# Kernel optimization log

Hardware: AMD Instinct MI355X
Metric: run time of the kernel (lower is better)

## Reference

```python
import jax, jax.numpy as jnp
import numpy as np

B, J, I = 16, 96, 96
E, H = 256, 512
VS, VT = 32000, 32000
MAX_JUMP = 96
SJ = 2 * MAX_JUMP + 1  # 193
ALPHA_P0 = 0.3


def _lstm(x, W, b, reverse=False):
    """TF LSTMCell (gate order i, j, f, o; forget_bias=1.0). x: [B,J,E] -> [B,J,H]."""
    h_dim = W.shape[1] // 4
    xs = jnp.swapaxes(x, 0, 1)  # [J,B,E]
    if reverse:
        xs = xs[::-1]

    def step(carry, xt):
        h, c = carry
        z = jnp.concatenate([xt, h], axis=-1) @ W + b  # [B,4H]
        i, g, f, o = jnp.split(z, 4, axis=-1)
        c = jax.nn.sigmoid(f + 1.0) * c + jax.nn.sigmoid(i) * jnp.tanh(g)
        h = jax.nn.sigmoid(o) * jnp.tanh(c)
        return (h, c), h

    init = (jnp.zeros((x.shape[0], h_dim), x.dtype), jnp.zeros((x.shape[0], h_dim), x.dtype))
    _, hs = jax.lax.scan(step, init, xs)
    if reverse:
        hs = hs[::-1]
    return jnp.swapaxes(hs, 0, 1)


def setup_inputs() -> dict:
    key = jax.random.key(0)
    ks = jax.random.split(key, 16)
    s = 0.05
    return {
        "sources": jax.random.randint(ks[0], (B, I), 0, VS, dtype=jnp.int32),
        "targets": jax.random.randint(ks[1], (B, J), 0, VT, dtype=jnp.int32),
        "targets_null": jnp.array([VT - 1], dtype=jnp.int32),
        "emb": jax.random.normal(ks[2], (VT, E), jnp.float32) * s,
        "W_fw": jax.random.normal(ks[3], (E + H, 4 * H), jnp.float32) * s,
        "b_fw": jnp.zeros((4 * H,), jnp.float32),
        "W_bw": jax.random.normal(ks[4], (E + H, 4 * H), jnp.float32) * s,
        "b_bw": jnp.zeros((4 * H,), jnp.float32),
        "W_lstm": jax.random.normal(ks[5], (2 * H, E), jnp.float32) * s,
        "W1": jax.random.normal(ks[6], (E, H), jnp.float32) * s,
        "b1": jnp.zeros((H,), jnp.float32),
        "Wv": jax.random.normal(ks[7], (H, VS), jnp.float32) * s,
        "bv": jnp.zeros((VS,), jnp.float32),
        "Wj": jax.random.normal(ks[8], (H, SJ), jnp.float32) * s,
        "bj": jnp.zeros((SJ,), jnp.float32),
        "Wp": jax.random.normal(ks[9], (H, 1), jnp.float32) * s,
        "bp": jnp.zeros((1,), jnp.float32),
    }


def reference(sources, targets, targets_null, emb, W_fw, b_fw, W_bw, b_bw,
              W_lstm, W1, b1, Wv, bv, Wj, bj, Wp, bp):
    # shared target encoder (emission & transition use the same variables)
    e_word = emb[targets]          # [B,J,E]
    e_null = emb[targets_null]     # [1,E]
    h_fw = _lstm(e_word, W_fw, b_fw, reverse=False)
    h_bw = _lstm(e_word, W_bw, b_bw, reverse=True)
    ts = jnp.concatenate([h_fw, h_bw], axis=-1) @ W_lstm   # [B,J,E]
    ts = jnp.tanh(ts @ W1 + b1)                            # [B,J,H]
    tn = jnp.tanh(e_null @ W1 + b1)                        # [1,H]
    # keep_prob = 1.0 -> dropout is identity

    # ---- emission ----
    p_word = jax.nn.softmax(ts @ Wv + bv, axis=-1)         # [B,J,VS]
    p_null = jax.nn.softmax(tn @ Wv + bv, axis=-1)         # [1,VS]
    em_word = jnp.take_along_axis(p_word, sources[:, None, :], axis=2)  # [B,J,I]
    em_null = jnp.broadcast_to(p_null[0][sources][:, None, :], em_word.shape)  # tile over J
    emission_prob = jnp.concatenate([em_word, em_null], axis=1)  # [B,2J,I]

    # ---- transition ----
    jw = jax.nn.softmax(ts @ Wj + bj, axis=-1)             # [B,J,SJ]
    p0_scalar = jax.nn.sigmoid(tn @ Wp + bp)[0, 0] * ALPHA_P0
    p0 = jnp.broadcast_to(p0_scalar, (targets.shape[0], targets.shape[1]))  # [B,J]

    j_idx = jnp.arange(J)
    # window indices: for target word j, gather jw[j, MAX_JUMP - j + i] for i in [0,J)
    idx = MAX_JUMP - j_idx[:, None] + j_idx[None, :]       # [J,J]
    jww = jnp.take_along_axis(jw, idx[None, :, :], axis=2)  # [B,J,J]
    jww_sum = jnp.sum(jww, axis=-1, keepdims=True)
    jww_n = jww * (1.0 - p0[:, :, None]) / jww_sum          # normalized non-null jumps

    eye = jnp.eye(J, dtype=jww.dtype)
    half = jnp.concatenate([jww_n, p0[:, :, None] * eye], axis=2)       # [B,J,2J]
    transition = jnp.concatenate([half, half], axis=1)                  # [B,2J,2J]
    lhalf = jnp.concatenate([jnp.log(jww_n), jnp.log(p0)[:, :, None] * eye], axis=2)
    transition_log = jnp.concatenate([lhalf, lhalf], axis=1)            # [B,2J,2J]

    return emission_prob, transition, transition_log
```

## Files before the change

kernel.cpp:

```cpp
#include <hip/hip_runtime.h>
#include <math.h>

#define B_ 16
#define J_ 96
#define I_ 96
#define E_ 256
#define H_ 512
#define VS_ 32000
#define SJ_ 193
#define NROW (B_*J_)

typedef __attribute__((ext_vector_type(8))) short short8;
typedef __attribute__((ext_vector_type(4))) float f32x4;
typedef __attribute__((ext_vector_type(4))) unsigned int u32x4;

__device__ __forceinline__ float sigf(float x){ return 1.f/(1.f+__expf(-x)); }

__device__ __forceinline__ unsigned short f2bf(float x){
  unsigned int u = __float_as_uint(x);
  unsigned int r = (u + 0x7FFFu + ((u>>16)&1u)) >> 16;
  return (unsigned short)r;
}
__device__ __forceinline__ float bf2f(unsigned short u){
  return __uint_as_float((unsigned int)u << 16);
}

#define ASYNC16(gp, lp) __builtin_amdgcn_global_load_lds( \
    (const __attribute__((address_space(1))) unsigned int*)(gp), \
    (__attribute__((address_space(3))) unsigned int*)(lp), 16, 0, 0)

__device__ __forceinline__ void wtr_tile256(const float* __restrict__ src,
                                            unsigned short* __restrict__ dst,
                                            int ldN, int nmax, int K, int n0, int k0,
                                            float* __restrict__ tile )
{
  const int t = threadIdx.x;
  #pragma unroll
  for (int rep = 0; rep < 16; rep++){
    int idx = rep*256 + t;
    int kk = idx >> 6, nn = idx & 63;
    tile[kk*65 + nn] = (n0+nn < nmax) ? src[(long long)(k0+kk)*ldN + n0 + nn] : 0.f;
  }
  __syncthreads();
  #pragma unroll
  for (int rep = 0; rep < 16; rep++){
    int idx = rep*256 + t;
    int nn = idx >> 6, kk = idx & 63;
    dst[(long long)(n0+nn)*K + k0 + kk] = f2bf(tile[kk*65 + nn]);
  }
}

__device__ __forceinline__ void wtr_tile(const float* __restrict__ src,
                                         unsigned short* __restrict__ dst,
                                         int ldN, int nmax, int K, int n0, int k0,
                                         float* __restrict__ tile)
{
  const int t = threadIdx.x;
  #pragma unroll
  for (int rep = 0; rep < 8; rep++){
    int idx = rep*512 + t;
    int kk = idx >> 6, nn = idx & 63;
    tile[kk*65 + nn] = (n0+nn < nmax) ? src[(long long)(k0+kk)*ldN + n0 + nn] : 0.f;
  }
  __syncthreads();
  #pragma unroll
  for (int rep = 0; rep < 8; rep++){
    int idx = rep*512 + t;
    int nn = idx >> 6, kk = idx & 63;
    dst[(long long)(n0+nn)*K + k0 + kk] = f2bf(tile[kk*65 + nn]);
  }
}

__global__ __launch_bounds__(256) void k_head(
    const int* __restrict__ targets, const float* __restrict__ emb,
    unsigned short* __restrict__ e_word_h,
    const float* __restrict__ Wfw, const float* __restrict__ Wbw,
    unsigned short* __restrict__ WT,
    unsigned int* __restrict__ hex, float* __restrict__ rowsum,
    const float* __restrict__ bfw, const float* __restrict__ bbw,
    float* __restrict__ wsb)
{
  __shared__ float tile[64*65];
  int bid = blockIdx.x;
  const int t = threadIdx.x;
  if (bid < 1536){
    int tr = targets[bid];
    e_word_h[(long long)bid*E_ + t] = f2bf(emb[(long long)tr*E_ + t]);
    return;
  }
  bid -= 1536;
  if (bid < 256){
    int y = bid >> 7;
    const float* src = y ? Wbw : Wfw;
    unsigned short* dst = WT + (long long)y*2048*256;
    int sid = bid & 127;
    wtr_tile256(src, dst, 2048, 2048, 256, (sid & 31)*64, (sid >> 5)*64, tile);
    return;
  }
  bid -= 256;
  if (bid < 128){ hex[bid*256 + t] = 0u; return; }
  bid -= 128;
  if (bid < 7){
    int i = bid*256 + t;
    if (i < NROW + 1) rowsum[i] = 0.f;
    return;
  }
  bid -= 7;
  int i = bid*256 + t;
  wsb[i] = (i < 2048) ? bfw[i] : bbw[i - 2048];
}

__device__ __forceinline__ void gemm128(const unsigned short* __restrict__ Ah,
                                        const unsigned short* __restrict__ Bh,
                                        int K, int m0, int n0,
                                        unsigned short* As, unsigned short* Bs,
                                        f32x4 (&acc)[4][4])
{
  const int t = threadIdx.x;
  const int lane = t & 63, w = t >> 6;
  const int wm = (w >> 1)*64, wn = (w & 1)*64;
  for (int k0 = 0; k0 < K; k0 += 64){
    #pragma unroll
    for (int p = 0; p < 4; p++){
      int rowA = p*32 + (t >> 3);
      int kc = (t & 7) ^ (rowA & 7);
      const unsigned short* ga = Ah + (long long)(m0 + rowA)*K + k0 + kc*8;
      const unsigned short* gb = Bh + (long long)(n0 + rowA)*K + k0 + kc*8;
      unsigned short* la = As + p*2048 + w*512;
      unsigned short* lb = Bs + p*2048 + w*512;
      ASYNC16(ga, la);
      ASYNC16(gb, lb);
    }
    __syncthreads();
    const int rr = lane & 15, kch = lane >> 4;
    #pragma unroll
    for (int kk = 0; kk < 2; kk++){
      short8 af[4], bf[4];
      #pragma unroll
      for (int mi = 0; mi < 4; mi++){
        int rowA = wm + mi*16 + rr;
        int slot = (kk*4 + kch) ^ (rowA & 7);
        af[mi] = *(const short8*)&As[rowA*64 + slot*8];
      }
      #pragma unroll
      for (int ni = 0; ni < 4; ni++){
        int rowB = wn + ni*16 + rr;
        int slot = (kk*4 + kch) ^ (rowB & 7);
        bf[ni] = *(const short8*)&Bs[rowB*64 + slot*8];
      }
      #pragma unroll
      for (int mi = 0; mi < 4; mi++)
        #pragma unroll
        for (int ni = 0; ni < 4; ni++)
          acc[mi][ni] = __builtin_amdgcn_mfma_f32_16x16x32_bf16(af[mi], bf[ni], acc[mi][ni], 0, 0, 0);
    }
    __syncthreads();
  }
}

template<int MODE>
__global__ __launch_bounds__(256, 2) void k_bgemm(
    const unsigned short* __restrict__ Ah,
    const unsigned short* __restrict__ Bh,
    int K, int ncols,
    const float* __restrict__ bias,
    float* __restrict__ Cf,
    unsigned short* __restrict__ Ch,
    int ldc,
    long long sB2, long long sBias2, long long sC2)
{
  __shared__ unsigned short As[128*64];
  __shared__ unsigned short Bs[128*64];
  if (blockIdx.y){
    Bh += sB2;
    if (bias) bias += sBias2;
    if (Cf) Cf += sC2;
    if (Ch) Ch += sC2;
  }
  int nwg = gridDim.x;
  int braw = blockIdx.x;
  int wg = (braw & 7)*(nwg >> 3) + (braw >> 3);
  int mt = wg % 12, nt = wg / 12;
  const int m0 = mt*128, n0 = nt*128;
  f32x4 acc[4][4] = {};
  gemm128(Ah, Bh, K, m0, n0, As, Bs, acc);
  const int t = threadIdx.x;
  const int lane = t & 63, w = t >> 6;
  const int wm = (w >> 1)*64, wn = (w & 1)*64;
  #pragma unroll
  for (int mi = 0; mi < 4; mi++){
    #pragma unroll
    for (int r = 0; r < 4; r++){
      int row = m0 + wm + mi*16 + ((lane >> 4) << 2) + r;
      #pragma unroll
      for (int ni = 0; ni < 4; ni++){
        int col = n0 + wn + ni*16 + (lane & 15);
        if (col >= ncols) continue;
        float v = acc[mi][ni][r] + (bias ? bias[col] : 0.f);
        if (MODE == 0){ Cf[(long long)row*ldc + col] = v; }
        if (MODE == 1){ Ch[(long long)row*ldc + col] = f2bf(v); }
        if (MODE == 2){
          v = tanhf(v);
          if (Cf) Cf[(long long)row*ldc + col] = v;
          Ch[(long long)row*ldc + col] = f2bf(v);
        }
      }
    }
  }
}

__global__ __launch_bounds__(512, 1) void k_fused(
    const unsigned short* __restrict__ Xh,
    const float* __restrict__ Wfw, const float* __restrict__ Wbw,
    unsigned int* __restrict__ hex32,
    unsigned short* __restrict__ Hcat_h,
    const int* __restrict__ tnull, const float* __restrict__ emb,
    const float* __restrict__ W1, const float* __restrict__ b1,
    const float* __restrict__ Wp, const float* __restrict__ bp,
    const float* __restrict__ Wv, const float* __restrict__ bv,
    unsigned short* __restrict__ WvT,
    float* __restrict__ lognull, float* __restrict__ nullsum,
    float* __restrict__ p0,
    const float* __restrict__ Wl, unsigned short* __restrict__ W_comboT,
    const float* __restrict__ Wj, unsigned short* __restrict__ WjT)
{
  __shared__ __align__(16) unsigned short W_s[64*512];
  __shared__ __align__(16) float z_s[2][8][16][68];
  const int bid = blockIdx.x;
  const int t = threadIdx.x;

  if (bid >= 64){
    float* zflat = &z_s[0][0][0][0];
    int sid = bid - 64;
    if (sid == 0){
      float* en  = zflat;
      float* red = zflat + 256;
      if (t < E_) en[t] = emb[(long long)tnull[0]*E_ + t];
      __syncthreads();
      float s = b1[t];
      for (int e = 0; e < E_; e++) s += en[e]*W1[(long long)e*H_ + t];
      red[t] = tanhf(s)*Wp[t];
      __syncthreads();
      for (int w = 256; w > 0; w >>= 1){
        if (t < w) red[t] += red[t+w];
        __syncthreads();
      }
      if (t == 0) p0[0] = sigf(red[0] + bp[0])*0.3f;
      return;
    }
    sid -= 1;
    if (sid < 128){
      const int K8 = sid*8;
      float* WlS = zflat;
      #pragma unroll
      for (int rep = 0; rep < 4; rep++){
        int id = rep*512 + t;
        int kl = id >> 8, e = id & 255;
        WlS[kl*256 + e] = Wl[(long long)(K8 + kl)*256 + e];
      }
      __syncthreads();
      float acc[8] = {};
      for (int e = 0; e < 256; e++){
        float w1v = W1[(long long)e*512 + t];
        #pragma unroll
        for (int j = 0; j < 8; j++) acc[j] += WlS[j*256 + e]*w1v;
      }
      #pragma unroll
      for (int j = 0; j < 8; j++)
        W_comboT[(long long)t*1024 + K8 + j] = f2bf(acc[j]);
      return;
    }
    sid -= 128;
    if (sid < 32){
      wtr_tile(Wj, WjT, SJ_, SJ_, 512, (sid & 3)*64, (sid >> 2)*64, zflat);
      return;
    }
    sid -= 32;
    if (sid < 63){
      float* en  = zflat;
      float* tns = zflat + 256;
      float* red = zflat + 768;
      if (t < E_) en[t] = emb[(long long)tnull[0]*E_ + t];
      __syncthreads();
      float s0 = b1[t];
      for (int e = 0; e < E_; e++) s0 += en[e]*W1[(long long)e*H_ + t];
      tns[t] = tanhf(s0);
      __syncthreads();
      int c = sid*512 + t;
      float p = 0.f;
      if (c < VS_){
        float s = bv[c];
        for (int k = 0; k < H_; k++) s += tns[k]*Wv[(long long)k*VS_ + c];
        lognull[c] = s;
        p = __expf(s);
      }
      red[t] = p;
      __syncthreads();
      for (int w = 256; w > 0; w >>= 1){
        if (t < w) red[t] += red[t+w];
        __syncthreads();
      }
      if (t == 0) atomicAdd(nullsum, red[0]);
      return;
    }
    sid -= 63;
    wtr_tile(Wv, WvT, VS_, VS_, H_, (sid % 500)*64, (sid / 500)*64, zflat);
    return;
  }

  const int dir = bid >> 5;
  const int slice = bid & 31;
  const int u0 = slice * 16;
  const int lane = t & 63;
  const int w = t >> 6;
  const int m = lane & 15, hi = lane >> 4;
  const unsigned short* X = Xh + (long long)dir*NROW*2048;
  const float* Wg = (dir ? Wbw : Wfw) + (long long)E_*2048;
  char* hexd = (char*)hex32 + dir*65536;

  for (int rep = 0; rep < 8; rep++){
    int id = rep*512 + t;
    int k = id >> 3, col8 = (id & 7)*8;
    int g = col8 >> 4, uu0 = col8 & 15;
    const float* src = Wg + (long long)k*2048 + g*512 + u0 + uu0;
    float4 w0 = *(const float4*)src;
    float4 w1 = *(const float4*)(src + 4);
    float wv8[8] = {w0.x,w0.y,w0.z,w0.w,w1.x,w1.y,w1.z,w1.w};
    #pragma unroll
    for (int j = 0; j < 8; j++){
      int c = col8 + j;
      int byte = (c << 10) + (k << 1);
      byte ^= ((c & 7) << 4);
      *(unsigned short*)((char*)W_s + byte) = f2bf(wv8[j]);
    }
  }
  __syncthreads();

  short8 bfr[4][2];
  #pragma unroll
  for (int nt = 0; nt < 4; nt++)
    #pragma unroll
    for (int ck = 0; ck < 2; ck++){
      int col = nt*16 + m;
      int kc = 2*w + ck;
      int byte = (col << 10) + kc*64 + hi*16;
      byte ^= ((col & 7) << 4);
      bfr[nt][ck] = *(const short8*)((const char*)W_s + byte);
    }

  const int eb = t >> 4, eu = t & 15;
  float creg = 0.f;

  for (int step = 0; step < J_; step++){
    const int par = step & 1;
    const int t_eff = dir ? (J_-1-step) : step;
    float xg0=0.f, xg1=0.f, xg2=0.f, xg3=0.f;
    if (t < 256){
      const unsigned short* xr = X + ((long long)eb*J_ + t_eff)*2048 + u0 + eu;
      xg0 = bf2f(xr[0]); xg1 = bf2f(xr[512]); xg2 = bf2f(xr[1024]); xg3 = bf2f(xr[1536]);
      asm volatile("" : "+v"(xg0), "+v"(xg1), "+v"(xg2), "+v"(xg3));
    }
    const char* ap = hexd + par*32768 + m*2048 + w*256 + hi*32;
    u32x4 d0, d1, d2, d3;
    const unsigned expt = (unsigned)step;
    unsigned spin = 0;
    for (;;){
      asm volatile("global_load_dwordx4 %0, %1, off sc0 sc1" : "=v"(d0) : "v"(ap));
      asm volatile("global_load_dwordx4 %0, %1, off offset:16 sc0 sc1" : "=v"(d1) : "v"(ap));
      asm volatile("global_load_dwordx4 %0, %1, off offset:128 sc0 sc1" : "=v"(d2) : "v"(ap));
      asm volatile("global_load_dwordx4 %0, %1, off offset:144 sc0 sc1" : "=v"(d3) : "v"(ap));
      asm volatile("s_waitcnt vmcnt(0)" ::: "memory");
      unsigned bad = (d0[1]^expt)|(d0[3]^expt)|(d1[1]^expt)|(d1[3]^expt)
                   | (d2[1]^expt)|(d2[3]^expt)|(d3[1]^expt)|(d3[3]^expt);
      if (__all(bad == 0u)) break;
      if (++spin > 65536u) break;
      __builtin_amdgcn_s_sleep(1);
    }
    __builtin_amdgcn_sched_barrier(0);
    union { unsigned int u[4]; short8 s; } a0, a1;
    a0.u[0]=d0[0]; a0.u[1]=d0[2]; a0.u[2]=d1[0]; a0.u[3]=d1[2];
    a1.u[0]=d2[0]; a1.u[1]=d2[2]; a1.u[2]=d3[0]; a1.u[3]=d3[2];
    f32x4 acc[4] = {{0.f,0.f,0.f,0.f},{0.f,0.f,0.f,0.f},{0.f,0.f,0.f,0.f},{0.f,0.f,0.f,0.f}};
    #pragma unroll
    for (int nt = 0; nt < 4; nt++){
      acc[nt] = __builtin_amdgcn_mfma_f32_16x16x32_bf16(a0.s, bfr[nt][0], acc[nt], 0,0,0);
      acc[nt] = __builtin_amdgcn_mfma_f32_16x16x32_bf16(a1.s, bfr[nt][1], acc[nt], 0,0,0);
    }
    #pragma unroll
    for (int nt = 0; nt < 4; nt++)
      #pragma unroll
      for (int r = 0; r < 4; r++)
        z_s[par][w][hi*4 + r][nt*16 + m] = acc[nt][r];
    __syncthreads();
    if (t < 256){
      float z0 = xg0, z1 = xg1, z2 = xg2, z3 = xg3;
      #pragma unroll
      for (int ke = 0; ke < 8; ke++){
        z0 += z_s[par][ke][eb][eu];
        z1 += z_s[par][ke][eb][16 + eu];
        z2 += z_s[par][ke][eb][32 + eu];
        z3 += z_s[par][ke][eb][48 + eu];
      }
      creg = sigf(z2 + 1.f)*creg + sigf(z0)*tanhf(z1);
      float hh = sigf(z3)*tanhf(creg);
      unsigned int hb16 = (unsigned int)f2bf(hh);
      unsigned int nb = (unsigned int)__shfl_xor((int)hb16, 1);
      if (!(eu & 1)){
        unsigned long long pkt = (unsigned long long)((hb16 & 0xffffu) | (nb << 16))
                               | ((unsigned long long)(unsigned)(step+1) << 32);
        __hip_atomic_store((unsigned long long*)(hexd + (par^1)*32768 + eb*2048 + (u0 + eu)*4),
                           pkt, __ATOMIC_RELAXED, __HIP_MEMORY_SCOPE_AGENT);
      }
      Hcat_h[((long long)eb*J_ + t_eff)*1024 + dir*512 + u0 + eu] = (unsigned short)hb16;
    }
  }
}

__global__ __launch_bounds__(256, 2) void k_mega(
    const unsigned short* __restrict__ t1h,
    const unsigned short* __restrict__ WvT,
    const unsigned short* __restrict__ WjT,
    const float* __restrict__ bv, const float* __restrict__ bj,
    const int* __restrict__ sources,
    float* __restrict__ rowsum, float* __restrict__ jlog,
    float* __restrict__ out_em)
{
  __shared__ unsigned short As[128*64];
  __shared__ unsigned short Bs[128*64];
  const int t = threadIdx.x;
  const int lane = t & 63, w = t >> 6;
  int bid = blockIdx.x;
  if (bid >= 3024){
    int tile = (bid - 3024)*4 + w;
    int b = tile / 36, tl = tile % 36;
    int mt = tl / 6, nt = tl % 6;
    const int rr = lane & 15, kq = lane >> 4;
    int s = sources[b*96 + nt*16 + rr];
    float bg = bv[s];
    const unsigned short* arow = t1h + ((long long)(b*96 + mt*16 + rr))*512 + kq*8;
    const unsigned short* brow = WvT + (long long)s*512 + kq*8;
    f32x4 acc = {0.f,0.f,0.f,0.f};
    #pragma unroll
    for (int kc = 0; kc < 16; kc++){
      short8 af = *(const short8*)(arow + kc*32);
      short8 bf = *(const short8*)(brow + kc*32);
      acc = __builtin_amdgcn_mfma_f32_16x16x32_bf16(af, bf, acc, 0, 0, 0);
    }
    #pragma unroll
    for (int r = 0; r < 4; r++){
      int j = mt*16 + kq*4 + r;
      int i = nt*16 + rr;
      out_em[((long long)b*192 + j)*96 + i] = __expf(acc[r] + bg);
    }
    return;
  }
  const bool isjl = (bid >= 3000);
  int m0, n0;
  const unsigned short* Bh;
  if (isjl){
    int idx = bid - 3000;
    m0 = (idx % 12)*128; n0 = (idx / 12)*128;
    Bh = WjT;
  } else {
    int wg = (bid & 7)*375 + (bid >> 3);
    m0 = (wg % 12)*128; n0 = (wg / 12)*128;
    Bh = WvT;
  }
  f32x4 acc[4][4] = {};
  gemm128(t1h, Bh, H_, m0, n0, As, Bs, acc);
  const int wm = (w >> 1)*64, wn = (w & 1)*64;
  #pragma unroll
  for (int mi = 0; mi < 4; mi++){
    #pragma unroll
    for (int r = 0; r < 4; r++){
      int row = m0 + wm + mi*16 + ((lane >> 4) << 2) + r;
      if (isjl){
        #pragma unroll
        for (int ni = 0; ni < 4; ni++){
          int col = n0 + wn + ni*16 + (lane & 15);
          if (col < SJ_) jlog[(long long)row*SJ_ + col] = acc[mi][ni][r] + bj[col];
        }
      } else {
        float s = 0.f;
        #pragma unroll
        for (int ni = 0; ni < 4; ni++){
          int col = n0 + wn + ni*16 + (lane & 15);
          s += __expf(acc[mi][ni][r] + bv[col]);
        }
        s += __shfl_xor(s, 1);
        s += __shfl_xor(s, 2);
        s += __shfl_xor(s, 4);
        s += __shfl_xor(s, 8);
        if ((lane & 15) == 0) atomicAdd(&rowsum[row], s);
      }
    }
  }
}

__global__ __launch_bounds__(128) void k_final(
    const float* __restrict__ jlog, const float* __restrict__ p0p,
    const float* __restrict__ rowsum,
    const float* __restrict__ lognull, const float* __restrict__ nullsum,
    const int* __restrict__ sources,
    float* __restrict__ out_em, float* __restrict__ T, float* __restrict__ TL)
{
  __shared__ float ex[128];
  __shared__ float red[128];
  int bx = blockIdx.x;
  int tid = threadIdx.x;
  if (bx >= NROW){
    int b = bx - NROW;
    if (tid < 96){
      int s = sources[b*96 + tid];
      float v = __expf(lognull[s]) / nullsum[0];
      for (int jj = 0; jj < 96; jj++)
        out_em[((long long)b*192 + 96 + jj)*96 + tid] = v;
    }
    return;
  }
  int b = bx / J_, j = bx % J_;
  float inv = 1.f / rowsum[bx];
  if (tid < 96)
    out_em[((long long)b*192 + j)*96 + tid] *= inv;
  float e = 0.f;
  if (tid < 96) e = __expf(jlog[(long long)bx*SJ_ + (96 - j + tid)]);
  ex[tid] = e; red[tid] = e;
  __syncthreads();
  for (int w = 64; w > 0; w >>= 1){
    if (tid < w) red[tid] += red[tid+w];
    __syncthreads();
  }
  float p0 = p0p[0];
  float scale = (1.f - p0) / red[0];
  float lp0 = logf(p0);
  long long r0 = ((long long)b*192 + j)*192;
  long long r1 = ((long long)b*192 + j + 96)*192;
  for (int col = tid; col < 192; col += 128){
    float tv, lv;
    if (col < 96){ tv = ex[col]*scale; lv = logf(tv); }
    else { bool d = (col - 96) == j; tv = d ? p0 : 0.f; lv = d ? lp0 : 0.f; }
    T[r0 + col] = tv; T[r1 + col] = tv;
    TL[r0 + col] = lv; TL[r1 + col] = lv;
  }
}

extern "C" void kernel_launch(void* const* d_in, const int* in_sizes, int n_in,
                              void* d_out, int out_size, void* d_ws, size_t ws_size,
                              hipStream_t stream)
{
  const int* sources = (const int*)d_in[0];
  const int* targets = (const int*)d_in[1];
  const int* tnull   = (const int*)d_in[2];
  const float* emb   = (const float*)d_in[3];
  const float* Wfw   = (const float*)d_in[4];
  const float* bfw   = (const float*)d_in[5];
  const float* Wbw   = (const float*)d_in[6];
  const float* bbw   = (const float*)d_in[7];
  const float* Wl    = (const float*)d_in[8];
  const float* W1    = (const float*)d_in[9];
  const float* b1    = (const float*)d_in[10];
  const float* Wv    = (const float*)d_in[11];
  const float* bv    = (const float*)d_in[12];
  const float* Wj    = (const float*)d_in[13];
  const float* bj    = (const float*)d_in[14];
  const float* Wp    = (const float*)d_in[15];
  const float* bp    = (const float*)d_in[16];
  float* out = (float*)d_out;
  float* ws  = (float*)d_ws;

  long long off = 0;
  unsigned short* Xh = (unsigned short*)(ws + off); off += 2LL*NROW*2048/2;
  unsigned short* e_word_h = (unsigned short*)(ws + off); off += (long long)NROW*E_/2;
  unsigned short* WT       = (unsigned short*)(ws + off); off += 2LL*2048*256/2;
  unsigned short* Hcat_h   = (unsigned short*)(ws + off); off += (long long)NROW*1024/2;
  unsigned int* hex32 = (unsigned int*)(ws + off); off += 32768;
  unsigned short* t1h = (unsigned short*)(ws + off); off += (long long)NROW*H_/2;
  unsigned short* W_comboT = (unsigned short*)(ws + off); off += 512LL*1024/2;
  unsigned short* WjT      = (unsigned short*)(ws + off); off += 256LL*512/2;
  float* rowsum = ws + off; off += NROW;
  float* nullsum= ws + off; off += 1;
  float* p0     = ws + off; off += 1;
  float* wsb    = ws + off; off += 4096;
  float* lognull= ws + off; off += VS_;
  float* jlog   = ws + off; off += (long long)NROW*SJ_;
  unsigned short* WvT = (unsigned short*)(ws + off); off += (long long)VS_*H_/2;

  float* out_em = out;
  float* out_T  = out + (long long)B_*192*96;
  float* out_TL = out_T + (long long)B_*192*192;

  k_head<<<1943, 256, 0, stream>>>(targets, emb, e_word_h, Wfw, Wbw, WT,
                                   hex32, rowsum, bfw, bbw, wsb);

  k_bgemm<1><<<dim3(192, 2), 256, 0, stream>>>(e_word_h, WT, E_, 2048, wsb,
                                               nullptr, Xh, 2048,
                                               2048LL*256, 2048LL, (long long)NROW*2048);

  k_fused<<<4288, 512, 0, stream>>>(Xh, Wfw, Wbw, hex32, Hcat_h,
                                    tnull, emb, W1, b1, Wp, bp, Wv, bv,
                                    WvT, lognull, nullsum, p0,
                                    Wl, W_comboT, Wj, WjT);

  k_bgemm<2><<<dim3(48, 1), 256, 0, stream>>>(Hcat_h, W_comboT, 2*H_, H_, b1,
                                              nullptr, t1h, H_, 0, 0, 0);

  k_mega<<<3168, 256, 0, stream>>>(t1h, WvT, WjT, bv, bj, sources,
                                   rowsum, jlog, out_em);

  k_final<<<NROW + B_, 128, 0, stream>>>(jlog, p0, rowsum, lognull, nullsum,
                                         sources, out_em, out_T, out_TL);
}
```

Measured before the change: 443.1 us.

## Halve LSTM recurrence blocks with wider per-block slices and fast gate math

```diff
diff --git a/kernel.cpp b/kernel.cpp
--- a/kernel.cpp
+++ b/kernel.cpp
@@ -14,15 +14,23 @@
 typedef __attribute__((ext_vector_type(4))) float f32x4;
 typedef __attribute__((ext_vector_type(4))) unsigned int u32x4;
 
-__device__ __forceinline__ float sigf(float x){ return 1.f/(1.f+__expf(-x)); }
+__device__ __forceinline__ float rcpfast(float x){
+  float r;
+  asm volatile("v_rcp_f32 %0, %1" : "=v"(r) : "v"(x));
+  return r;
+}
+__device__ __forceinline__ float sigfast(float x){
+  return rcpfast(1.f + __expf(-x));
+}
+__device__ __forceinline__ float tanhfast(float x){
+  float e = __expf(2.f*x);
+  return 1.f - 2.f*rcpfast(e + 1.f);
+}
 
 __device__ __forceinline__ unsigned short f2bf(float x){
   unsigned int u = __float_as_uint(x);
   unsigned int r = (u + 0x7FFFu + ((u>>16)&1u)) >> 16;
   return (unsigned short)r;
-}
-__device__ __forceinline__ float bf2f(unsigned short u){
-  return __uint_as_float((unsigned int)u << 16);
 }
 
 #define ASYNC16(gp, lp) __builtin_amdgcn_global_load_lds( \
@@ -198,7 +206,6 @@
         if (col >= ncols) continue;
         float v = acc[mi][ni][r] + (bias ? bias[col] : 0.f);
         if (MODE == 0){ Cf[(long long)row*ldc + col] = v; }
-        if (MODE == 1){ Ch[(long long)row*ldc + col] = f2bf(v); }
         if (MODE == 2){
           v = tanhf(v);
           if (Cf) Cf[(long long)row*ldc + col] = v;
@@ -210,7 +217,7 @@
 }
 
 __global__ __launch_bounds__(512, 1) void k_fused(
-    const unsigned short* __restrict__ Xh,
+    const float* __restrict__ Xfw, const float* __restrict__ Xbw,
     const float* __restrict__ Wfw, const float* __restrict__ Wbw,
     unsigned int* __restrict__ hex32,
     unsigned short* __restrict__ Hcat_h,
@@ -224,14 +231,13 @@
     const float* __restrict__ Wl, unsigned short* __restrict__ W_comboT,
     const float* __restrict__ Wj, unsigned short* __restrict__ WjT)
 {
-  __shared__ __align__(16) unsigned short W_s[64*512];
-  __shared__ __align__(16) float z_s[2][8][16][68];
+  __shared__ __align__(16) float z_s[2][8][16][132];
   const int bid = blockIdx.x;
   const int t = threadIdx.x;
 
-  if (bid >= 64){
+  if (bid >= 32){
     float* zflat = &z_s[0][0][0][0];
-    int sid = bid - 64;
+    int sid = bid - 32;
     if (sid == 0){
       float* en  = zflat;
       float* red = zflat + 256;
@@ -245,7 +251,7 @@
         if (t < w) red[t] += red[t+w];
         __syncthreads();
       }
-      if (t == 0) p0[0] = sigf(red[0] + bp[0])*0.3f;
+      if (t == 0) p0[0] = sigfast(red[0] + bp[0])*0.3f;
       return;
     }
     sid -= 1;
@@ -308,58 +314,41 @@
     return;
   }
 
-  const int dir = bid >> 5;
-  const int slice = bid & 31;
-  const int u0 = slice * 16;
+  const int dir = bid >> 4;
+  const int slice = bid & 15;
+  const int u0 = slice * 32;
   const int lane = t & 63;
   const int w = t >> 6;
   const int m = lane & 15, hi = lane >> 4;
-  const unsigned short* X = Xh + (long long)dir*NROW*2048;
+  const float* X = dir ? Xbw : Xfw;
   const float* Wg = (dir ? Wbw : Wfw) + (long long)E_*2048;
   char* hexd = (char*)hex32 + dir*65536;
 
-  for (int rep = 0; rep < 8; rep++){
-    int id = rep*512 + t;
-    int k = id >> 3, col8 = (id & 7)*8;
-    int g = col8 >> 4, uu0 = col8 & 15;
-    const float* src = Wg + (long long)k*2048 + g*512 + u0 + uu0;
-    float4 w0 = *(const float4*)src;
-    float4 w1 = *(const float4*)(src + 4);
-    float wv8[8] = {w0.x,w0.y,w0.z,w0.w,w1.x,w1.y,w1.z,w1.w};
-    #pragma unroll
-    for (int j = 0; j < 8; j++){
-      int c = col8 + j;
-      int byte = (c << 10) + (k << 1);
-      byte ^= ((c & 7) << 4);
-      *(unsigned short*)((char*)W_s + byte) = f2bf(wv8[j]);
-    }
-  }
-  __syncthreads();
-
-  short8 bfr[4][2];
+  short8 bfr[8][2];
   #pragma unroll
-  for (int nt = 0; nt < 4; nt++)
+  for (int nt = 0; nt < 8; nt++){
+    int c = nt*16 + m;
+    int gcol = (c >> 5)*512 + u0 + (c & 31);
     #pragma unroll
     for (int ck = 0; ck < 2; ck++){
-      int col = nt*16 + m;
-      int kc = 2*w + ck;
-      int byte = (col << 10) + kc*64 + hi*16;
-      byte ^= ((col & 7) << 4);
-      bfr[nt][ck] = *(const short8*)((const char*)W_s + byte);
-    }
-
-  const int eb = t >> 4, eu = t & 15;
+      int kbase = (2*w + ck)*32 + hi*8;
+      union { short s[8]; short8 v; } tmp;
+      #pragma unroll
+      for (int j = 0; j < 8; j++)
+        tmp.s[j] = (short)f2bf(Wg[(long long)(kbase + j)*2048 + gcol]);
+      bfr[nt][ck] = tmp.v;
+    }
+  }
+
+  const int eb = t >> 5, eu = t & 31;
   float creg = 0.f;
 
   for (int step = 0; step < J_; step++){
     const int par = step & 1;
     const int t_eff = dir ? (J_-1-step) : step;
-    float xg0=0.f, xg1=0.f, xg2=0.f, xg3=0.f;
-    if (t < 256){
-      const unsigned short* xr = X + ((long long)eb*J_ + t_eff)*2048 + u0 + eu;
-      xg0 = bf2f(xr[0]); xg1 = bf2f(xr[512]); xg2 = bf2f(xr[1024]); xg3 = bf2f(xr[1536]);
-      asm volatile("" : "+v"(xg0), "+v"(xg1), "+v"(xg2), "+v"(xg3));
-    }
+    const float* xr = X + ((long long)eb*J_ + t_eff)*2048 + u0 + eu;
+    float xg0 = xr[0], xg1 = xr[512], xg2 = xr[1024], xg3 = xr[1536];
+    asm volatile("" : "+v"(xg0), "+v"(xg1), "+v"(xg2), "+v"(xg3));
     const char* ap = hexd + par*32768 + m*2048 + w*256 + hi*32;
     u32x4 d0, d1, d2, d3;
     const unsigned expt = (unsigned)step;
@@ -380,29 +369,29 @@
     union { unsigned int u[4]; short8 s; } a0, a1;
     a0.u[0]=d0[0]; a0.u[1]=d0[2]; a0.u[2]=d1[0]; a0.u[3]=d1[2];
     a1.u[0]=d2[0]; a1.u[1]=d2[2]; a1.u[2]=d3[0]; a1.u[3]=d3[2];
-    f32x4 acc[4] = {{0.f,0.f,0.f,0.f},{0.f,0.f,0.f,0.f},{0.f,0.f,0.f,0.f},{0.f,0.f,0.f,0.f}};
-    #pragma unroll
-    for (int nt = 0; nt < 4; nt++){
+    f32x4 acc[8] = {};
+    #pragma unroll
+    for (int nt = 0; nt < 8; nt++){
       acc[nt] = __builtin_amdgcn_mfma_f32_16x16x32_bf16(a0.s, bfr[nt][0], acc[nt], 0,0,0);
       acc[nt] = __builtin_amdgcn_mfma_f32_16x16x32_bf16(a1.s, bfr[nt][1], acc[nt], 0,0,0);
     }
     #pragma unroll
-    for (int nt = 0; nt < 4; nt++)
+    for (int nt = 0; nt < 8; nt++)
       #pragma unroll
       for (int r = 0; r < 4; r++)
         z_s[par][w][hi*4 + r][nt*16 + m] = acc[nt][r];
     __syncthreads();
-    if (t < 256){
+    {
       float z0 = xg0, z1 = xg1, z2 = xg2, z3 = xg3;
       #pragma unroll
       for (int ke = 0; ke < 8; ke++){
         z0 += z_s[par][ke][eb][eu];
-        z1 += z_s[par][ke][eb][16 + eu];
-        z2 += z_s[par][ke][eb][32 + eu];
-        z3 += z_s[par][ke][eb][48 + eu];
-      }
-      creg = sigf(z2 + 1.f)*creg + sigf(z0)*tanhf(z1);
-      float hh = sigf(z3)*tanhf(creg);
+        z1 += z_s[par][ke][eb][32 + eu];
+        z2 += z_s[par][ke][eb][64 + eu];
+        z3 += z_s[par][ke][eb][96 + eu];
+      }
+      creg = sigfast(z2 + 1.f)*creg + sigfast(z0)*tanhfast(z1);
+      float hh = sigfast(z3)*tanhfast(creg);
       unsigned int hb16 = (unsigned int)f2bf(hh);
       unsigned int nb = (unsigned int)__shfl_xor((int)hb16, 1);
       if (!(eu & 1)){
@@ -569,7 +558,8 @@
   float* ws  = (float*)d_ws;
 
   long long off = 0;
-  unsigned short* Xh = (unsigned short*)(ws + off); off += 2LL*NROW*2048/2;
+  float* Xfw    = ws + off; off += (long long)NROW*2048;
+  float* Xbw    = ws + off; off += (long long)NROW*2048;
   unsigned short* e_word_h = (unsigned short*)(ws + off); off += (long long)NROW*E_/2;
   unsigned short* WT       = (unsigned short*)(ws + off); off += 2LL*2048*256/2;
   unsigned short* Hcat_h   = (unsigned short*)(ws + off); off += (long long)NROW*1024/2;
@@ -592,11 +582,11 @@
   k_head<<<1943, 256, 0, stream>>>(targets, emb, e_word_h, Wfw, Wbw, WT,
                                    hex32, rowsum, bfw, bbw, wsb);
 
-  k_bgemm<1><<<dim3(192, 2), 256, 0, stream>>>(e_word_h, WT, E_, 2048, wsb,
-                                               nullptr, Xh, 2048,
+  k_bgemm<0><<<dim3(192, 2), 256, 0, stream>>>(e_word_h, WT, E_, 2048, wsb,
+                                               Xfw, nullptr, 2048,
                                                2048LL*256, 2048LL, (long long)NROW*2048);
 
-  k_fused<<<4288, 512, 0, stream>>>(Xh, Wfw, Wbw, hex32, Hcat_h,
+  k_fused<<<4256, 512, 0, stream>>>(Xfw, Xbw, Wfw, Wbw, hex32, Hcat_h,
                                     tnull, emb, W1, b1, Wp, bp, Wv, bv,
                                     WvT, lognull, nullsum, p0,
                                     Wl, W_comboT, Wj, WjT);
```

After: 395.5 us, median of 2. 1.12x faster.
